# Kernel optimization log

Measured on AMD Instinct MI355X. Metric: run time of the kernel, lower is better.

The kernel has to match this reference:

```python
import jax, jax.numpy as jnp
import numpy as np

TOP_P = 0.9
NEG_FILL = -100000.0
POS_FILL = 100000.0


def setup_inputs() -> dict:
    key = jax.random.key(0)
    k1, k2, k3 = jax.random.split(key, 3)
    B, S, V = 256, 128, 128000
    input_ids = jax.random.randint(k1, (B, S), 0, V, dtype=jnp.int64)
    logits = jax.random.normal(k2, (B, V), dtype=jnp.float32)
    # uniform watermark keys xi in (0,1); avoid exact 0 for log
    xi = jax.random.uniform(k3, (V,), dtype=jnp.float32, minval=1e-6, maxval=1.0)
    return {"input_ids": input_ids, "logits": logits, "xi": xi}


def reference(input_ids, logits, xi):
    B, V = logits.shape
    probs = jax.nn.softmax(logits, axis=-1)                       # [B, V]
    order = jnp.argsort(-probs, axis=-1)                          # descending sort indices [B, V]
    sorted_probs = jnp.take_along_axis(probs, order, axis=-1)     # [B, V]
    cum = jnp.cumsum(sorted_probs, axis=-1)                       # [B, V]
    # torch.searchsorted(cum, top_p, right=False) == count of cum < top_p
    cutoff = jnp.sum(cum < TOP_P, axis=-1)                        # [B]
    keep = jnp.arange(V)[None, :] <= cutoff[:, None]              # keep [:cutoff+1]
    # exponential-minimum trick: argmin over -log(xi)/p within the top-p set
    scores = -jnp.log(xi[order]) / sorted_probs                   # [B, V]
    scores = jnp.where(keep, scores, jnp.inf)
    pos = jnp.argmin(scores, axis=-1)                             # [B]
    next_token = jnp.take_along_axis(order, pos[:, None], axis=-1)[:, 0]  # [B]
    out = jnp.full_like(logits, NEG_FILL)
    out = out.at[jnp.arange(B), next_token].set(POS_FILL)
    return out
```

## Files before the change

### kernel.cpp

```cpp
#include <hip/hip_runtime.h>
#include <hip/hip_bf16.h>
#include <math.h>


constexpr int   NBINS     = 4096;
constexpr float BIN_MIN   = -8.0f;
constexpr float BIN_SCALE = 256.0f;
constexpr float BIN_OFF   = 2048.0f;
constexpr float BIN_W     = 1.0f / 256.0f;
constexpr int   BINB_CAP  = 512;
constexpr int   MAXC      = 96;
constexpr float CAND_THR  = -3.0f;
constexpr float NEG_FILL  = -100000.0f;
constexpr float POS_FILL  =  100000.0f;
constexpr float TOPP      = 0.9f;
constexpr int   BPR_FILL  = 32;
constexpr int   SLICES    = 8;

struct Ws {
    float*    key;
    unsigned* candIdx;
    float*    candKey;
    int*      candCnt;
    unsigned* phist;
    float*    lmaxArr;
    unsigned long long* winner;
};

__device__ __forceinline__ unsigned sortable(float f) {
    unsigned u = __float_as_uint(f);
    return (u & 0x80000000u) ? ~u : (u | 0x80000000u);
}
__device__ __forceinline__ int binOf(float l) {
    int b = (int)fmaf(l, BIN_SCALE, BIN_OFF);
    return min(max(b, 0), NBINS - 1);
}

__global__ __launch_bounds__(256)
void k0_keys(const float4* __restrict__ xi4, float* __restrict__ key,
             unsigned* __restrict__ candIdx, float* __restrict__ candKey,
             int* __restrict__ candCnt, int V4)
{
    __shared__ int cnt;
    __shared__ unsigned sIdx[MAXC];
    __shared__ float    sKey[MAXC];
    if (threadIdx.x == 0) cnt = 0;
    __syncthreads();

    const int f = blockIdx.x * 256 + threadIdx.x;
    if (f < V4) {
        float4 x = xi4[f];
        float kv[4];
        kv[0] = __logf(-__logf(x.x));
        kv[1] = __logf(-__logf(x.y));
        kv[2] = __logf(-__logf(x.z));
        kv[3] = __logf(-__logf(x.w));
        reinterpret_cast<float4*>(key)[f] = make_float4(kv[0], kv[1], kv[2], kv[3]);
        #pragma unroll
        for (int c = 0; c < 4; ++c) {
            if (kv[c] < CAND_THR) {
                int p = atomicAdd(&cnt, 1);
                if (p < MAXC) { sIdx[p] = (unsigned)(f * 4 + c); sKey[p] = kv[c]; }
            }
        }
    }
    __syncthreads();
    const int base = blockIdx.x * MAXC;
    const int n = min(cnt, MAXC);
    for (int i = threadIdx.x; i < MAXC; i += 256) {
        candIdx[base + i] = (i < n) ? sIdx[i] : 0u;
        candKey[base + i] = (i < n) ? sKey[i] : INFINITY;
    }
    if (threadIdx.x == 0) candCnt[blockIdx.x] = cnt;
}

__global__ __launch_bounds__(256, 8)
void k1_sweep(const float* __restrict__ logits, unsigned* __restrict__ phist,
              float* __restrict__ lmaxArr, int V)
{
    const int row = blockIdx.x / SLICES;
    const int sl  = blockIdx.x % SLICES;
    const int n4  = V >> 2;
    const int per = n4 / SLICES;
    const float4* p4 = reinterpret_cast<const float4*>(logits + (size_t)row * V) + sl * per;

    __shared__ unsigned lh[NBINS];
    __shared__ float wrf[4];
    for (int i = threadIdx.x; i < NBINS; i += 256) lh[i] = 0u;
    __syncthreads();

    float lmax = -INFINITY;
    for (int base = 0; base < per; base += 1024) {
        float4 r[4];
        int    j[4];
        #pragma unroll
        for (int u = 0; u < 4; ++u) {
            j[u] = base + u * 256 + threadIdx.x;
            if (j[u] < per) r[u] = p4[j[u]];
        }
        #pragma unroll
        for (int u = 0; u < 4; ++u) {
            if (j[u] < per) {
                float lv[4] = {r[u].x, r[u].y, r[u].z, r[u].w};
                #pragma unroll
                for (int c = 0; c < 4; ++c) {
                    atomicAdd(&lh[binOf(lv[c])], 1u);
                    lmax = fmaxf(lmax, lv[c]);
                }
            }
        }
    }
    __syncthreads();

    unsigned* dst = phist + ((size_t)row * SLICES + sl) * NBINS;
    uint4* d4 = reinterpret_cast<uint4*>(dst);
    const uint4* s4 = reinterpret_cast<const uint4*>(lh);
    for (int i = threadIdx.x; i < NBINS / 4; i += 256) d4[i] = s4[i];

    for (int off = 32; off >= 1; off >>= 1)
        lmax = fmaxf(lmax, __shfl_down(lmax, off));
    if ((threadIdx.x & 63) == 0) wrf[threadIdx.x >> 6] = lmax;
    __syncthreads();
    if (threadIdx.x == 0) {
        float m = fmaxf(fmaxf(wrf[0], wrf[1]), fmaxf(wrf[2], wrf[3]));
        lmaxArr[row * SLICES + sl] = m;
    }
}

__device__ __forceinline__ void scan_bins(const unsigned* lh, int lane,
                                          int& candBin, double& candS, double& target)
{
    const int hi = NBINS - 1 - (lane << 6);
    double seg = 0.0;
    for (int k = 0; k < 64; ++k) {
        int b = hi - k;
        seg += (double)lh[b] * (double)__expf(fmaf((float)b + 0.5f, BIN_W, BIN_MIN));
    }
    double v = seg;
    for (int off = 1; off < 64; off <<= 1) {
        double u = __shfl_up(v, off);
        if (lane >= off) v += u;
    }
    double excl = v - seg;
    double total = __shfl(v, 63);
    target = TOPP * total;

    candBin = -1; candS = 0.0;
    double cum = excl;
    for (int k = 0; k < 64; ++k) {
        int b = hi - k;
        double h = (double)lh[b] * (double)__expf(fmaf((float)b + 0.5f, BIN_W, BIN_MIN));
        if (candBin < 0 && cum + h >= target) { candBin = b; candS = cum; }
        cum += h;
    }
    for (int off = 32; off >= 1; off >>= 1) {
        int    ob = __shfl_xor(candBin, off);
        double os = __shfl_xor(candS, off);
        if (ob > candBin) { candBin = ob; candS = os; }
    }
}

__global__ __launch_bounds__(1024)
void k2_resolve(const float* __restrict__ logits, const float* __restrict__ key,
                const unsigned* __restrict__ phist, const float* __restrict__ lmaxArr,
                const unsigned* __restrict__ candIdx, const float* __restrict__ candKey,
                const int* __restrict__ candCnt,
                unsigned long long* __restrict__ winner,
                int V, int nchunk, int nslots)
{
    const int row = blockIdx.x;
    const int tid = threadIdx.x;
    const int n4  = V >> 2;
    const float* rowp = logits + (size_t)row * V;
    const float4* p4 = reinterpret_cast<const float4*>(rowp);

    __shared__ unsigned lh[NBINS];
    __shared__ float  s_bl[BINB_CAP];
    __shared__ int    s_bi[BINB_CAP];
    __shared__ float  s_sl[BINB_CAP];
    __shared__ int    s_si[BINB_CAP];
    __shared__ double s_be[BINB_CAP];
    __shared__ unsigned long long wrd[16];
    __shared__ int   sB2, sB, sNeedFull;
    __shared__ float sLcut;
    __shared__ int   sIcut;
    __shared__ double sCumAbove, sTarget;
    __shared__ unsigned long long sBest;

    const unsigned* ph = phist + (size_t)row * SLICES * NBINS;
    for (int i = tid; i < NBINS; i += 1024) {
        unsigned s = 0;
        #pragma unroll
        for (int k = 0; k < SLICES; ++k) s += ph[k * NBINS + i];
        lh[i] = s;
    }
    if (tid == 0) { sB2 = 0; sNeedFull = 0; }
    __syncthreads();
    if (tid < nchunk && candCnt[tid] > MAXC) atomicOr(&sNeedFull, 1);

    if (tid < 64) {
        int b; double cs, tg;
        scan_bins(lh, tid, b, cs, tg);
        if (tid == 0) { sB = b; sCumAbove = cs; sTarget = tg; }
    }
    __syncthreads();
    const int B = sB;

    for (int base = 0; base < n4; base += 4096) {
        float4 r[4];
        int    j[4];
        #pragma unroll
        for (int u = 0; u < 4; ++u) {
            j[u] = base + u * 1024 + tid;
            if (j[u] < n4) r[u] = p4[j[u]];
        }
        #pragma unroll
        for (int u = 0; u < 4; ++u) {
            if (j[u] < n4) {
                float lv[4] = {r[u].x, r[u].y, r[u].z, r[u].w};
                #pragma unroll
                for (int c = 0; c < 4; ++c) {
                    if (binOf(lv[c]) == B) {
                        int q = atomicAdd(&sB2, 1);
                        if (q < BINB_CAP) { s_bl[q] = lv[c]; s_bi[q] = j[u] * 4 + c; }
                    }
                }
            }
        }
    }
    __syncthreads();
    const int nB = min(sB2, BINB_CAP);

    for (int i = tid; i < nB; i += 1024) {
        float li = s_bl[i]; int ii = s_bi[i];
        int r = 0;
        for (int j = 0; j < nB; ++j) {
            float lj = s_bl[j]; int ij = s_bi[j];
            r += (lj > li) || (lj == li && ij < ii);
        }
        s_sl[r] = li; s_si[r] = ii;
    }
    __syncthreads();

    for (int i = tid; i < nB; i += 1024) s_be[i] = exp((double)s_sl[i]);
    __syncthreads();
    if (tid == 0) {
        double cum = sCumAbove, target = sTarget;
        int m = nB;
        for (int k = 0; k < nB; ++k) {
            cum += s_be[k];
            if (cum >= target) { m = k + 1; break; }
        }
        m = max(m, 1);
        if (nB == 0) { sNeedFull = 1; sLcut = (float)B * BIN_W + BIN_MIN; sIcut = 0x7fffffff; }
        else { sLcut = s_sl[m - 1]; sIcut = s_si[m - 1]; }
    }
    __syncthreads();
    const float lcut = sLcut;
    const int   icut = sIcut;

    unsigned long long best = ~0ull;
    for (int s = tid; s < nslots; s += 1024) {
        unsigned idx = candIdx[s];
        float ck = candKey[s];
        float l = rowp[idx];
        bool kept = (l > lcut) || (l == lcut && (int)idx <= icut);
        if (kept) {
            unsigned long long pack =
                ((unsigned long long)sortable(ck - l) << 32) | idx;
            best = pack < best ? pack : best;
        }
    }
    for (int off = 32; off >= 1; off >>= 1) {
        unsigned long long o = __shfl_down(best, off);
        best = o < best ? o : best;
    }
    if ((tid & 63) == 0) wrd[tid >> 6] = best;
    __syncthreads();
    if (tid == 0) {
        unsigned long long b = wrd[0];
        for (int w = 1; w < 16; ++w) b = wrd[w] < b ? wrd[w] : b;
        sBest = b;
        float lmax = -INFINITY;
        for (int k = 0; k < SLICES; ++k) lmax = fmaxf(lmax, lmaxArr[row * SLICES + k]);
        unsigned bound = sortable(CAND_THR - lmax);
        if (!((unsigned)(b >> 32) < bound)) sNeedFull = 1;
    }
    __syncthreads();

    if (sNeedFull) {
        for (int j = tid; j < V; j += 1024) {
            float l = rowp[j];
            bool kept = (l > lcut) || (l == lcut && j <= icut);
            if (kept) {
                unsigned long long pack =
                    ((unsigned long long)sortable(key[j] - l) << 32) | (unsigned)j;
                best = pack < best ? pack : best;
            }
        }
        for (int off = 32; off >= 1; off >>= 1) {
            unsigned long long o = __shfl_down(best, off);
            best = o < best ? o : best;
        }
        if ((tid & 63) == 0) wrd[tid >> 6] = best;
        __syncthreads();
        if (tid == 0) {
            unsigned long long b = sBest;
            for (int w = 0; w < 16; ++w) b = wrd[w] < b ? wrd[w] : b;
            sBest = b;
        }
        __syncthreads();
    }

    if (tid == 0) winner[row] = sBest;
}

__global__ __launch_bounds__(256)
void kd_fill(float* __restrict__ out,
             const unsigned long long* __restrict__ winner, int V)
{
    const int row = blockIdx.x / BPR_FILL;
    const int seg = blockIdx.x % BPR_FILL;
    const int n4  = V >> 2;
    const int per = n4 / BPR_FILL;
    const int start = seg * per;
    const int end = (seg == BPR_FILL - 1) ? n4 : start + per;
    float4* o4 = reinterpret_cast<float4*>(out + (size_t)row * V);

    const unsigned win = (unsigned)(winner[row] & 0xffffffffu);
    const int winj = (int)(win >> 2);

    const float4 nf = make_float4(NEG_FILL, NEG_FILL, NEG_FILL, NEG_FILL);
    for (int j = start + threadIdx.x; j < end; j += 256) {
        float4 v = nf;
        if (j == winj) {
            float ov[4] = {v.x, v.y, v.z, v.w};
            ov[win & 3] = POS_FILL;
            v = make_float4(ov[0], ov[1], ov[2], ov[3]);
        }
        o4[j] = v;
    }
}

extern "C" void kernel_launch(void* const* d_in, const int* in_sizes, int n_in,
                              void* d_out, int out_size, void* d_ws, size_t ws_size,
                              hipStream_t stream) {
    const float* logits = (const float*)d_in[1];
    const float* xi     = (const float*)d_in[2];
    float*       out    = (float*)d_out;
    const int V = in_sizes[2];
    const int B = in_sizes[1] / V;
    const int V4 = V / 4;
    const int nchunk = (V + 1023) / 1024;
    const int nslots = nchunk * MAXC;

    char* w = (char*)d_ws;
    size_t off = 0;
    Ws ws;
    ws.key     = (float*)(w + off);    off += (size_t)V * sizeof(float);
    off = (off + 255) & ~(size_t)255;
    ws.candIdx = (unsigned*)(w + off); off += (size_t)nslots * sizeof(unsigned);
    ws.candKey = (float*)(w + off);    off += (size_t)nslots * sizeof(float);
    ws.candCnt = (int*)(w + off);      off += (size_t)nchunk * sizeof(int);
    off = (off + 255) & ~(size_t)255;
    ws.phist   = (unsigned*)(w + off); off += (size_t)B * SLICES * NBINS * sizeof(unsigned);
    ws.lmaxArr = (float*)(w + off);    off += (size_t)B * SLICES * sizeof(float);
    off = (off + 255) & ~(size_t)255;
    ws.winner  = (unsigned long long*)(w + off); off += (size_t)B * sizeof(unsigned long long);

    k0_keys   <<<(V4 + 255) / 256, 256, 0, stream>>>((const float4*)xi, ws.key,
                                                     ws.candIdx, ws.candKey, ws.candCnt, V4);
    k1_sweep  <<<B * SLICES, 256, 0, stream>>>(logits, ws.phist, ws.lmaxArr, V);
    k2_resolve<<<B, 1024, 0, stream>>>(logits, ws.key, ws.phist, ws.lmaxArr,
                                       ws.candIdx, ws.candKey, ws.candCnt,
                                       ws.winner, V, nchunk, nslots);
    kd_fill   <<<B * BPR_FILL, 256, 0, stream>>>(out, ws.winner, V);
}
```

Baseline: 320.4 us.

## Replace histogram top-p search with windowed stash and single logits pass

The per-slice 4096-bin histogram is replaced by per-slice totals of exp mass, the mass above a fixed logit window, and a shared-memory stash of logits that fall inside a narrow window around the expected top-p cutoff. The resolve kernel then finds the cutoff from the stashed elements only, instead of rereading every logits row. A full-row histogram fallback covers the case where the cutoff falls outside the window or a stash overflows. Slice-level candidate minima from the low-key xi set are computed in the sweep. The output fill becomes a separate grid-stride kernel, and the resolve kernel scatters only the winning token. This removes a second full read of the logits. In exchange the sweep does an expf and double accumulation per element, and speed relies on the window matching the logits distribution.

```diff
diff --git a/kernel.cpp b/kernel.cpp
--- a/kernel.cpp
+++ b/kernel.cpp
@@ -3,127 +3,175 @@
 #include <math.h>
 
 
-constexpr int   NBINS     = 4096;
-constexpr float BIN_MIN   = -8.0f;
-constexpr float BIN_SCALE = 256.0f;
-constexpr float BIN_OFF   = 2048.0f;
-constexpr float BIN_W     = 1.0f / 256.0f;
-constexpr int   BINB_CAP  = 512;
-constexpr int   MAXC      = 96;
-constexpr float CAND_THR  = -3.0f;
-constexpr float NEG_FILL  = -100000.0f;
-constexpr float POS_FILL  =  100000.0f;
-constexpr float TOPP      = 0.9f;
-constexpr int   BPR_FILL  = 32;
-constexpr int   SLICES    = 8;
+constexpr int   SLICES   = 8;
+constexpr int   STCAP    = 2048;
+constexpr int   CCAP     = 1024;
+constexpr int   WBINS    = 64;
+constexpr float WLO      = -0.40625f;
+constexpr float WHI      = -0.15625f;
+constexpr float WSCALE   = 256.0f;
+constexpr int   BINB_CAP = 768;
+constexpr float CAND_THR = -3.0f;
+constexpr float NEG_FILL = -100000.0f;
+constexpr float POS_FILL =  100000.0f;
+constexpr float TOPP     = 0.9f;
+constexpr int   NBINS    = 4096;
+constexpr float BIN_MIN  = -8.0f;
+constexpr float BIN_SCALE= 256.0f;
+constexpr float BIN_OFF  = 2048.0f;
+constexpr float BIN_W    = 1.0f / 256.0f;
 
 struct Ws {
     float*    key;
-    unsigned* candIdx;
-    float*    candKey;
+    uint2*    cand;
     int*      candCnt;
-    unsigned* phist;
+    uint2*    stash;
+    int*      stashCnt;
+    double*   totArr;
+    double*   abvArr;
     float*    lmaxArr;
-    unsigned long long* winner;
+    unsigned long long* sliceBest;
 };
 
 __device__ __forceinline__ unsigned sortable(float f) {
     unsigned u = __float_as_uint(f);
     return (u & 0x80000000u) ? ~u : (u | 0x80000000u);
 }
+__device__ __forceinline__ unsigned long long fxmass(float l) {
+    return (unsigned long long)((double)__expf(l) * 4294967296.0);
+}
 __device__ __forceinline__ int binOf(float l) {
     int b = (int)fmaf(l, BIN_SCALE, BIN_OFF);
     return min(max(b, 0), NBINS - 1);
 }
 
 __global__ __launch_bounds__(256)
+void kd_neg(float4* __restrict__ out4, long total4)
+{
+    const long stride = (long)gridDim.x * 256;
+    const float4 nf = make_float4(NEG_FILL, NEG_FILL, NEG_FILL, NEG_FILL);
+    for (long i = (long)blockIdx.x * 256 + threadIdx.x; i < total4; i += stride)
+        out4[i] = nf;
+}
+
+__global__ __launch_bounds__(1024)
 void k0_keys(const float4* __restrict__ xi4, float* __restrict__ key,
-             unsigned* __restrict__ candIdx, float* __restrict__ candKey,
-             int* __restrict__ candCnt, int V4)
+             uint2* __restrict__ cand, int* __restrict__ candCnt, int V)
 {
+    const int seg = blockIdx.x;
+    const int st4 = (V / SLICES) >> 2;
+    const int base4 = seg * st4;
     __shared__ int cnt;
-    __shared__ unsigned sIdx[MAXC];
-    __shared__ float    sKey[MAXC];
+    __shared__ uint2 cl[CCAP];
     if (threadIdx.x == 0) cnt = 0;
     __syncthreads();
 
-    const int f = blockIdx.x * 256 + threadIdx.x;
-    if (f < V4) {
-        float4 x = xi4[f];
+    for (int i = threadIdx.x; i < st4; i += 1024) {
+        float4 x = xi4[base4 + i];
         float kv[4];
         kv[0] = __logf(-__logf(x.x));
         kv[1] = __logf(-__logf(x.y));
         kv[2] = __logf(-__logf(x.z));
         kv[3] = __logf(-__logf(x.w));
-        reinterpret_cast<float4*>(key)[f] = make_float4(kv[0], kv[1], kv[2], kv[3]);
+        reinterpret_cast<float4*>(key)[base4 + i] =
+            make_float4(kv[0], kv[1], kv[2], kv[3]);
         #pragma unroll
         for (int c = 0; c < 4; ++c) {
             if (kv[c] < CAND_THR) {
                 int p = atomicAdd(&cnt, 1);
-                if (p < MAXC) { sIdx[p] = (unsigned)(f * 4 + c); sKey[p] = kv[c]; }
-            }
-        }
-    }
-    __syncthreads();
-    const int base = blockIdx.x * MAXC;
-    const int n = min(cnt, MAXC);
-    for (int i = threadIdx.x; i < MAXC; i += 256) {
-        candIdx[base + i] = (i < n) ? sIdx[i] : 0u;
-        candKey[base + i] = (i < n) ? sKey[i] : INFINITY;
-    }
-    if (threadIdx.x == 0) candCnt[blockIdx.x] = cnt;
+                if (p < CCAP)
+                    cl[p] = make_uint2((unsigned)((base4 + i) * 4 + c),
+                                       __float_as_uint(kv[c]));
+            }
+        }
+    }
+    __syncthreads();
+    const int n = min(cnt, CCAP);
+    for (int i = threadIdx.x; i < CCAP; i += 1024)
+        cand[seg * CCAP + i] = (i < n) ? cl[i] : make_uint2(0u, 0x7f800000u);
+    if (threadIdx.x == 0) candCnt[seg] = cnt;
 }
 
 __global__ __launch_bounds__(256, 8)
-void k1_sweep(const float* __restrict__ logits, unsigned* __restrict__ phist,
-              float* __restrict__ lmaxArr, int V)
+void k1_sweep(const float* __restrict__ logits, Ws ws, int V)
 {
     const int row = blockIdx.x / SLICES;
     const int sl  = blockIdx.x % SLICES;
-    const int n4  = V >> 2;
-    const int per = n4 / SLICES;
-    const float4* p4 = reinterpret_cast<const float4*>(logits + (size_t)row * V) + sl * per;
-
-    __shared__ unsigned lh[NBINS];
-    __shared__ float wrf[4];
-    for (int i = threadIdx.x; i < NBINS; i += 256) lh[i] = 0u;
-    __syncthreads();
-
+    const int st4 = (V / SLICES) >> 2;
+    const float* rowp = logits + (size_t)row * V;
+    const float4* p4 = reinterpret_cast<const float4*>(rowp) + (size_t)sl * st4;
+    const int gbase = sl * st4 * 4;
+
+    __shared__ uint2 ss[STCAP];
+    __shared__ int scnt;
+    __shared__ double wrT[4], wrA[4];
+    __shared__ float  wrL[4];
+    __shared__ unsigned long long wrB[4];
+    if (threadIdx.x == 0) scnt = 0;
+    __syncthreads();
+
+    double tot = 0.0, abv = 0.0;
     float lmax = -INFINITY;
-    for (int base = 0; base < per; base += 1024) {
-        float4 r[4];
-        int    j[4];
+    for (int j = threadIdx.x; j < st4; j += 256) {
+        float4 r = p4[j];
+        float lv[4] = {r.x, r.y, r.z, r.w};
         #pragma unroll
-        for (int u = 0; u < 4; ++u) {
-            j[u] = base + u * 256 + threadIdx.x;
-            if (j[u] < per) r[u] = p4[j[u]];
-        }
-        #pragma unroll
-        for (int u = 0; u < 4; ++u) {
-            if (j[u] < per) {
-                float lv[4] = {r[u].x, r[u].y, r[u].z, r[u].w};
-                #pragma unroll
-                for (int c = 0; c < 4; ++c) {
-                    atomicAdd(&lh[binOf(lv[c])], 1u);
-                    lmax = fmaxf(lmax, lv[c]);
-                }
-            }
-        }
-    }
-    __syncthreads();
-
-    unsigned* dst = phist + ((size_t)row * SLICES + sl) * NBINS;
-    uint4* d4 = reinterpret_cast<uint4*>(dst);
-    const uint4* s4 = reinterpret_cast<const uint4*>(lh);
-    for (int i = threadIdx.x; i < NBINS / 4; i += 256) d4[i] = s4[i];
-
-    for (int off = 32; off >= 1; off >>= 1)
+        for (int c = 0; c < 4; ++c) {
+            float l = lv[c];
+            float e = __expf(l);
+            tot += (double)e;
+            abv += (l >= WHI) ? (double)e : 0.0;
+            lmax = fmaxf(lmax, l);
+            if (l >= WLO && l < WHI) {
+                int p = atomicAdd(&scnt, 1);
+                if (p < STCAP)
+                    ss[p] = make_uint2(__float_as_uint(l),
+                                       (unsigned)(gbase + j * 4 + c));
+            }
+        }
+    }
+
+    unsigned long long best = ~0ull;
+    const int cn = min(ws.candCnt[sl], CCAP);
+    const uint2* cl = ws.cand + sl * CCAP;
+    for (int i = threadIdx.x; i < cn; i += 256) {
+        uint2 c = cl[i];
+        float l = rowp[c.x];
+        if (l >= WHI) {
+            float sc = __uint_as_float(c.y) - l;
+            unsigned long long pack =
+                ((unsigned long long)sortable(sc) << 32) | c.x;
+            best = pack < best ? pack : best;
+        }
+    }
+    __syncthreads();
+
+    const int n = min(scnt, STCAP);
+    uint2* dst = ws.stash + ((size_t)row * SLICES + sl) * STCAP;
+    for (int i = threadIdx.x; i < n; i += 256) dst[i] = ss[i];
+
+    for (int off = 32; off >= 1; off >>= 1) {
+        tot += __shfl_down(tot, off);
+        abv += __shfl_down(abv, off);
         lmax = fmaxf(lmax, __shfl_down(lmax, off));
-    if ((threadIdx.x & 63) == 0) wrf[threadIdx.x >> 6] = lmax;
+        unsigned long long o = __shfl_down(best, off);
+        best = o < best ? o : best;
+    }
+    const int wv = threadIdx.x >> 6;
+    if ((threadIdx.x & 63) == 0) {
+        wrT[wv] = tot; wrA[wv] = abv; wrL[wv] = lmax; wrB[wv] = best;
+    }
     __syncthreads();
     if (threadIdx.x == 0) {
-        float m = fmaxf(fmaxf(wrf[0], wrf[1]), fmaxf(wrf[2], wrf[3]));
-        lmaxArr[row * SLICES + sl] = m;
+        double T = 0.0, A = 0.0; float L = -INFINITY;
+        unsigned long long Bt = ~0ull;
+        for (int w = 0; w < 4; ++w) {
+            T += wrT[w]; A += wrA[w]; L = fmaxf(L, wrL[w]);
+            Bt = wrB[w] < Bt ? wrB[w] : Bt;
+        }
+        const int s = row * SLICES + sl;
+        ws.totArr[s] = T; ws.abvArr[s] = A; ws.lmaxArr[s] = L;
+        ws.sliceBest[s] = Bt; ws.stashCnt[s] = scnt;
     }
 }
 
@@ -161,185 +209,245 @@
 }
 
 __global__ __launch_bounds__(1024)
-void k2_resolve(const float* __restrict__ logits, const float* __restrict__ key,
-                const unsigned* __restrict__ phist, const float* __restrict__ lmaxArr,
-                const unsigned* __restrict__ candIdx, const float* __restrict__ candKey,
-                const int* __restrict__ candCnt,
-                unsigned long long* __restrict__ winner,
-                int V, int nchunk, int nslots)
+void k2_resolve(const float* __restrict__ logits, float* __restrict__ out,
+                Ws ws, int V)
 {
     const int row = blockIdx.x;
     const int tid = threadIdx.x;
-    const int n4  = V >> 2;
     const float* rowp = logits + (size_t)row * V;
-    const float4* p4 = reinterpret_cast<const float4*>(rowp);
-
-    __shared__ unsigned lh[NBINS];
-    __shared__ float  s_bl[BINB_CAP];
-    __shared__ int    s_bi[BINB_CAP];
-    __shared__ float  s_sl[BINB_CAP];
-    __shared__ int    s_si[BINB_CAP];
-    __shared__ double s_be[BINB_CAP];
+    const float* key = ws.key;
+
+    __shared__ unsigned long long massFx[WBINS];
+    __shared__ float s_bl[BINB_CAP];
+    __shared__ int   s_bi[BINB_CAP];
+    __shared__ float s_sl[BINB_CAP];
+    __shared__ int   s_si[BINB_CAP];
+    __shared__ unsigned fbhist[NBINS];
     __shared__ unsigned long long wrd[16];
-    __shared__ int   sB2, sB, sNeedFull;
-    __shared__ float sLcut;
+    __shared__ int   sB2, sB, sNeedB, sNeedA;
+    __shared__ float sLcut, sLmax;
     __shared__ int   sIcut;
-    __shared__ double sCumAbove, sTarget;
-    __shared__ unsigned long long sBest;
-
-    const unsigned* ph = phist + (size_t)row * SLICES * NBINS;
-    for (int i = tid; i < NBINS; i += 1024) {
-        unsigned s = 0;
-        #pragma unroll
-        for (int k = 0; k < SLICES; ++k) s += ph[k * NBINS + i];
-        lh[i] = s;
-    }
-    if (tid == 0) { sB2 = 0; sNeedFull = 0; }
-    __syncthreads();
-    if (tid < nchunk && candCnt[tid] > MAXC) atomicOr(&sNeedFull, 1);
-
-    if (tid < 64) {
-        int b; double cs, tg;
-        scan_bins(lh, tid, b, cs, tg);
-        if (tid == 0) { sB = b; sCumAbove = cs; sTarget = tg; }
-    }
-    __syncthreads();
-    const int B = sB;
-
-    for (int base = 0; base < n4; base += 4096) {
-        float4 r[4];
-        int    j[4];
-        #pragma unroll
-        for (int u = 0; u < 4; ++u) {
-            j[u] = base + u * 1024 + tid;
-            if (j[u] < n4) r[u] = p4[j[u]];
-        }
-        #pragma unroll
-        for (int u = 0; u < 4; ++u) {
-            if (j[u] < n4) {
-                float lv[4] = {r[u].x, r[u].y, r[u].z, r[u].w};
-                #pragma unroll
-                for (int c = 0; c < 4; ++c) {
-                    if (binOf(lv[c]) == B) {
-                        int q = atomicAdd(&sB2, 1);
-                        if (q < BINB_CAP) { s_bl[q] = lv[c]; s_bi[q] = j[u] * 4 + c; }
-                    }
+    __shared__ double sCumAboveB, sTarget;
+    __shared__ unsigned long long sBestHi, sBest;
+
+    if (tid == 0) {
+        double T = 0.0, A = 0.0; float L = -INFINITY;
+        unsigned long long Bt = ~0ull;
+        int needB = 0, needA = 0;
+        for (int k = 0; k < SLICES; ++k) {
+            const int s = row * SLICES + k;
+            T += ws.totArr[s]; A += ws.abvArr[s];
+            L = fmaxf(L, ws.lmaxArr[s]);
+            unsigned long long v = ws.sliceBest[s];
+            Bt = v < Bt ? v : Bt;
+            if (ws.stashCnt[s] > STCAP) needB = 1;
+            if (ws.candCnt[k] > CCAP)   needA = 1;
+        }
+        sTarget = (double)TOPP * T;
+        sLmax = L; sBestHi = Bt;
+        sNeedB = needB; sNeedA = needA;
+        sCumAboveB = A;
+        sB2 = 0;
+    }
+    for (int i = tid; i < WBINS; i += 1024) massFx[i] = 0ull;
+    __syncthreads();
+
+    for (int k = 0; k < SLICES; ++k) {
+        const int s = row * SLICES + k;
+        const int n = min(ws.stashCnt[s], STCAP);
+        const uint2* sp = ws.stash + (size_t)s * STCAP;
+        for (int i = tid; i < n; i += 1024) {
+            float l = __uint_as_float(sp[i].x);
+            int wb = (int)floorf((l - WLO) * WSCALE);
+            wb = min(max(wb, 0), WBINS - 1);
+            atomicAdd(&massFx[wb], fxmass(l));
+        }
+    }
+    __syncthreads();
+
+    if (tid == 0) {
+        double cum = sCumAboveB;
+        const double target = sTarget;
+        if (cum >= target) sNeedB = 1;
+        else {
+            int B = -1; double ca = 0.0;
+            for (int b = WBINS - 1; b >= 0; --b) {
+                double m = (double)massFx[b] * 0x1p-32;
+                if (cum + m >= target) { B = b; ca = cum; break; }
+                cum += m;
+            }
+            if (B < 0) sNeedB = 1;
+            else { sB = B; sCumAboveB = ca; }
+        }
+    }
+    __syncthreads();
+
+    if (!sNeedB) {
+        const int B = sB;
+        for (int k = 0; k < SLICES; ++k) {
+            const int s = row * SLICES + k;
+            const int n = min(ws.stashCnt[s], STCAP);
+            const uint2* sp = ws.stash + (size_t)s * STCAP;
+            for (int i = tid; i < n; i += 1024) {
+                float l = __uint_as_float(sp[i].x);
+                int wb = (int)floorf((l - WLO) * WSCALE);
+                wb = min(max(wb, 0), WBINS - 1);
+                if (wb == B) {
+                    int q = atomicAdd(&sB2, 1);
+                    if (q < BINB_CAP) { s_bl[q] = l; s_bi[q] = (int)sp[i].y; }
                 }
             }
         }
-    }
-    __syncthreads();
-    const int nB = min(sB2, BINB_CAP);
-
-    for (int i = tid; i < nB; i += 1024) {
-        float li = s_bl[i]; int ii = s_bi[i];
-        int r = 0;
-        for (int j = 0; j < nB; ++j) {
-            float lj = s_bl[j]; int ij = s_bi[j];
-            r += (lj > li) || (lj == li && ij < ii);
-        }
-        s_sl[r] = li; s_si[r] = ii;
-    }
-    __syncthreads();
-
-    for (int i = tid; i < nB; i += 1024) s_be[i] = exp((double)s_sl[i]);
-    __syncthreads();
-    if (tid == 0) {
-        double cum = sCumAbove, target = sTarget;
-        int m = nB;
-        for (int k = 0; k < nB; ++k) {
-            cum += s_be[k];
-            if (cum >= target) { m = k + 1; break; }
-        }
-        m = max(m, 1);
-        if (nB == 0) { sNeedFull = 1; sLcut = (float)B * BIN_W + BIN_MIN; sIcut = 0x7fffffff; }
-        else { sLcut = s_sl[m - 1]; sIcut = s_si[m - 1]; }
-    }
-    __syncthreads();
-    const float lcut = sLcut;
-    const int   icut = sIcut;
+        __syncthreads();
+        const int nB = min(sB2, BINB_CAP);
+        if (sB2 > BINB_CAP && tid == 0) sNeedB = 1;
+        __syncthreads();
+        if (!sNeedB) {
+            for (int i = tid; i < nB; i += 1024) {
+                float li = s_bl[i]; int ii = s_bi[i];
+                int r = 0;
+                for (int j = 0; j < nB; ++j) {
+                    float lj = s_bl[j]; int ij = s_bi[j];
+                    r += (lj > li) || (lj == li && ij < ii);
+                }
+                s_sl[r] = li; s_si[r] = ii;
+            }
+            __syncthreads();
+            if (tid == 0) {
+                double cum = sCumAboveB;
+                const double target = sTarget;
+                int m = nB;
+                for (int k = 0; k < nB; ++k) {
+                    cum += (double)fxmass(s_sl[k]) * 0x1p-32;
+                    if (cum >= target) { m = k + 1; break; }
+                }
+                m = max(m, 1);
+                sLcut = s_sl[m - 1];
+                sIcut = s_si[m - 1];
+            }
+            __syncthreads();
+        }
+    }
 
     unsigned long long best = ~0ull;
-    for (int s = tid; s < nslots; s += 1024) {
-        unsigned idx = candIdx[s];
-        float ck = candKey[s];
-        float l = rowp[idx];
-        bool kept = (l > lcut) || (l == lcut && (int)idx <= icut);
-        if (kept) {
-            unsigned long long pack =
-                ((unsigned long long)sortable(ck - l) << 32) | idx;
-            best = pack < best ? pack : best;
-        }
-    }
-    for (int off = 32; off >= 1; off >>= 1) {
-        unsigned long long o = __shfl_down(best, off);
-        best = o < best ? o : best;
-    }
-    if ((tid & 63) == 0) wrd[tid >> 6] = best;
-    __syncthreads();
-    if (tid == 0) {
-        unsigned long long b = wrd[0];
-        for (int w = 1; w < 16; ++w) b = wrd[w] < b ? wrd[w] : b;
-        sBest = b;
-        float lmax = -INFINITY;
-        for (int k = 0; k < SLICES; ++k) lmax = fmaxf(lmax, lmaxArr[row * SLICES + k]);
-        unsigned bound = sortable(CAND_THR - lmax);
-        if (!((unsigned)(b >> 32) < bound)) sNeedFull = 1;
-    }
-    __syncthreads();
-
-    if (sNeedFull) {
+    if (!sNeedB) {
+        const float lcut = sLcut; const int icut = sIcut;
+        for (int k = 0; k < SLICES; ++k) {
+            const int s = row * SLICES + k;
+            const int n = min(ws.stashCnt[s], STCAP);
+            const uint2* sp = ws.stash + (size_t)s * STCAP;
+            for (int i = tid; i < n; i += 1024) {
+                float l = __uint_as_float(sp[i].x);
+                int idx = (int)sp[i].y;
+                bool kept = (l > lcut) || (l == lcut && idx <= icut);
+                if (kept) {
+                    float sc = key[idx] - l;
+                    unsigned long long pack =
+                        ((unsigned long long)sortable(sc) << 32) | (unsigned)idx;
+                    best = pack < best ? pack : best;
+                }
+            }
+        }
+        for (int off = 32; off >= 1; off >>= 1) {
+            unsigned long long o = __shfl_down(best, off);
+            best = o < best ? o : best;
+        }
+        if ((tid & 63) == 0) wrd[tid >> 6] = best;
+        __syncthreads();
+        if (tid == 0) {
+            unsigned long long b = sBestHi;
+            for (int w = 0; w < 16; ++w) b = wrd[w] < b ? wrd[w] : b;
+            sBest = b;
+            unsigned bound = sortable(CAND_THR - sLmax);
+            if (!((unsigned)(b >> 32) < bound)) sNeedA = 1;
+        }
+        __syncthreads();
+    }
+
+    if (sNeedB) {
+        for (int i = tid; i < NBINS; i += 1024) fbhist[i] = 0u;
+        if (tid == 0) sB2 = 0;
+        __syncthreads();
+        const int n4 = V >> 2;
+        const float4* p4 = reinterpret_cast<const float4*>(rowp);
+        for (int j = tid; j < n4; j += 1024) {
+            float4 r = p4[j];
+            atomicAdd(&fbhist[binOf(r.x)], 1u);
+            atomicAdd(&fbhist[binOf(r.y)], 1u);
+            atomicAdd(&fbhist[binOf(r.z)], 1u);
+            atomicAdd(&fbhist[binOf(r.w)], 1u);
+        }
+        __syncthreads();
+        if (tid < 64) {
+            int b; double cs, tg;
+            scan_bins(fbhist, tid, b, cs, tg);
+            if (tid == 0) { sB = b; sCumAboveB = cs; sTarget = tg; }
+        }
+        __syncthreads();
+        const int B = sB;
+        for (int j = tid; j < V; j += 1024) {
+            float l = rowp[j];
+            if (binOf(l) == B) {
+                int q = atomicAdd(&sB2, 1);
+                if (q < BINB_CAP) { s_bl[q] = l; s_bi[q] = j; }
+            }
+        }
+        __syncthreads();
+        const int nB = min(sB2, BINB_CAP);
+        for (int i = tid; i < nB; i += 1024) {
+            float li = s_bl[i]; int ii = s_bi[i];
+            int r = 0;
+            for (int j = 0; j < nB; ++j) {
+                float lj = s_bl[j]; int ij = s_bi[j];
+                r += (lj > li) || (lj == li && ij < ii);
+            }
+            s_sl[r] = li; s_si[r] = ii;
+        }
+        __syncthreads();
+        if (tid == 0) {
+            double cum = sCumAboveB;
+            const double target = sTarget;
+            int m = nB;
+            for (int k = 0; k < nB; ++k) {
+                cum += (double)fxmass(s_sl[k]) * 0x1p-32;
+                if (cum >= target) { m = k + 1; break; }
+            }
+            m = max(m, 1);
+            if (nB == 0) { sLcut = (float)B * BIN_W + BIN_MIN; sIcut = 0x7fffffff; }
+            else { sLcut = s_sl[m - 1]; sIcut = s_si[m - 1]; }
+            sNeedA = 1;
+        }
+        __syncthreads();
+    }
+
+    if (sNeedA) {
+        const float lcut = sLcut; const int icut = sIcut;
+        unsigned long long fb = ~0ull;
         for (int j = tid; j < V; j += 1024) {
             float l = rowp[j];
             bool kept = (l > lcut) || (l == lcut && j <= icut);
             if (kept) {
                 unsigned long long pack =
                     ((unsigned long long)sortable(key[j] - l) << 32) | (unsigned)j;
-                best = pack < best ? pack : best;
+                fb = pack < fb ? pack : fb;
             }
         }
         for (int off = 32; off >= 1; off >>= 1) {
-            unsigned long long o = __shfl_down(best, off);
-            best = o < best ? o : best;
-        }
-        if ((tid & 63) == 0) wrd[tid >> 6] = best;
+            unsigned long long o = __shfl_down(fb, off);
+            fb = o < fb ? o : fb;
+        }
+        if ((tid & 63) == 0) wrd[tid >> 6] = fb;
         __syncthreads();
         if (tid == 0) {
-            unsigned long long b = sBest;
+            unsigned long long b = ~0ull;
             for (int w = 0; w < 16; ++w) b = wrd[w] < b ? wrd[w] : b;
             sBest = b;
         }
         __syncthreads();
     }
 
-    if (tid == 0) winner[row] = sBest;
-}
-
-__global__ __launch_bounds__(256)
-void kd_fill(float* __restrict__ out,
-             const unsigned long long* __restrict__ winner, int V)
-{
-    const int row = blockIdx.x / BPR_FILL;
-    const int seg = blockIdx.x % BPR_FILL;
-    const int n4  = V >> 2;
-    const int per = n4 / BPR_FILL;
-    const int start = seg * per;
-    const int end = (seg == BPR_FILL - 1) ? n4 : start + per;
-    float4* o4 = reinterpret_cast<float4*>(out + (size_t)row * V);
-
-    const unsigned win = (unsigned)(winner[row] & 0xffffffffu);
-    const int winj = (int)(win >> 2);
-
-    const float4 nf = make_float4(NEG_FILL, NEG_FILL, NEG_FILL, NEG_FILL);
-    for (int j = start + threadIdx.x; j < end; j += 256) {
-        float4 v = nf;
-        if (j == winj) {
-            float ov[4] = {v.x, v.y, v.z, v.w};
-            ov[win & 3] = POS_FILL;
-            v = make_float4(ov[0], ov[1], ov[2], ov[3]);
-        }
-        o4[j] = v;
-    }
+    if (tid == 0)
+        out[(size_t)row * V + (unsigned)(sBest & 0xffffffffu)] = POS_FILL;
 }
 
 extern "C" void kernel_launch(void* const* d_in, const int* in_sizes, int n_in,
@@ -350,29 +458,28 @@
     float*       out    = (float*)d_out;
     const int V = in_sizes[2];
     const int B = in_sizes[1] / V;
-    const int V4 = V / 4;
-    const int nchunk = (V + 1023) / 1024;
-    const int nslots = nchunk * MAXC;
 
     char* w = (char*)d_ws;
     size_t off = 0;
     Ws ws;
-    ws.key     = (float*)(w + off);    off += (size_t)V * sizeof(float);
+    ws.key       = (float*)(w + off);  off += (size_t)V * sizeof(float);
     off = (off + 255) & ~(size_t)255;
-    ws.candIdx = (unsigned*)(w + off); off += (size_t)nslots * sizeof(unsigned);
-    ws.candKey = (float*)(w + off);    off += (size_t)nslots * sizeof(float);
-    ws.candCnt = (int*)(w + off);      off += (size_t)nchunk * sizeof(int);
+    ws.cand      = (uint2*)(w + off);  off += (size_t)SLICES * CCAP * sizeof(uint2);
+    ws.candCnt   = (int*)(w + off);    off += (size_t)SLICES * sizeof(int);
     off = (off + 255) & ~(size_t)255;
-    ws.phist   = (unsigned*)(w + off); off += (size_t)B * SLICES * NBINS * sizeof(unsigned);
-    ws.lmaxArr = (float*)(w + off);    off += (size_t)B * SLICES * sizeof(float);
+    ws.stash     = (uint2*)(w + off);  off += (size_t)B * SLICES * STCAP * sizeof(uint2);
+    ws.stashCnt  = (int*)(w + off);    off += (size_t)B * SLICES * sizeof(int);
     off = (off + 255) & ~(size_t)255;
-    ws.winner  = (unsigned long long*)(w + off); off += (size_t)B * sizeof(unsigned long long);
-
-    k0_keys   <<<(V4 + 255) / 256, 256, 0, stream>>>((const float4*)xi, ws.key,
-                                                     ws.candIdx, ws.candKey, ws.candCnt, V4);
-    k1_sweep  <<<B * SLICES, 256, 0, stream>>>(logits, ws.phist, ws.lmaxArr, V);
-    k2_resolve<<<B, 1024, 0, stream>>>(logits, ws.key, ws.phist, ws.lmaxArr,
-                                       ws.candIdx, ws.candKey, ws.candCnt,
-                                       ws.winner, V, nchunk, nslots);
-    kd_fill   <<<B * BPR_FILL, 256, 0, stream>>>(out, ws.winner, V);
-}
+    ws.totArr    = (double*)(w + off); off += (size_t)B * SLICES * sizeof(double);
+    ws.abvArr    = (double*)(w + off); off += (size_t)B * SLICES * sizeof(double);
+    ws.lmaxArr   = (float*)(w + off);  off += (size_t)B * SLICES * sizeof(float);
+    off = (off + 255) & ~(size_t)255;
+    ws.sliceBest = (unsigned long long*)(w + off); off += (size_t)B * SLICES * sizeof(unsigned long long);
+
+    const long total4 = (long)B * V / 4;
+    kd_neg    <<<2048, 256, 0, stream>>>((float4*)out, total4);
+    k0_keys   <<<SLICES, 1024, 0, stream>>>((const float4*)xi, ws.key,
+                                            ws.cand, ws.candCnt, V);
+    k1_sweep  <<<B * SLICES, 256, 0, stream>>>(logits, ws, V);
+    k2_resolve<<<B, 1024, 0, stream>>>(logits, out, ws, V);
+}
```

Result: slower. 328.1 us (+2.4%).
